# Optimization experiments

Hardware: AMD Instinct MI355X
Metric: run time of the kernel (lower is better)

The kernel has to match this reference:

```python
import jax, jax.numpy as jnp
import numpy as np

BATCH, ENC_IN, D_MODEL, D_STATE = 16, 256, 256, 16


def _mamba_params(key, d, d_conv, prefix):
    di = 2 * d  # expand = 2
    dtr = max(d // 16, 1)  # dt_rank = ceil(d_model/16)
    ks = jax.random.split(key, 6)
    return {
        prefix + '_in_w': jax.random.normal(ks[0], (2 * di, d), jnp.float32) * 0.02,
        prefix + '_conv_w': jax.random.normal(ks[1], (di, d_conv), jnp.float32) * 0.1,
        prefix + '_conv_b': jnp.zeros((di,), jnp.float32),
        prefix + '_xproj_w': jax.random.normal(ks[2], (dtr + 2 * D_STATE, di), jnp.float32) * 0.02,
        prefix + '_dt_w': jax.random.normal(ks[3], (di, dtr), jnp.float32) * 0.02,
        prefix + '_dt_b': jax.random.normal(ks[4], (di,), jnp.float32) * 0.02,
        prefix + '_Alog': jnp.log(jnp.broadcast_to(jnp.arange(1, D_STATE + 1, dtype=jnp.float32), (di, D_STATE))),
        prefix + '_Dp': jnp.ones((di,), jnp.float32),
        prefix + '_out_w': jax.random.normal(ks[5], (d, di), jnp.float32) * 0.02,
    }


def setup_inputs() -> dict:
    key = jax.random.key(0)
    k0, k1, k2, k3 = jax.random.split(key, 4)
    inp = {
        'x': jax.random.normal(k0, (BATCH, ENC_IN, D_MODEL), jnp.float32),
        'ln_g': jnp.ones((D_MODEL,), jnp.float32),
        'ln_b': jnp.zeros((D_MODEL,), jnp.float32),
    }
    inp.update(_mamba_params(k1, D_MODEL, 1, 'mf'))  # channel mixer fwd, d_conv=1
    inp.update(_mamba_params(k2, D_MODEL, 1, 'mb'))  # channel mixer bwd, d_conv=1
    inp.update(_mamba_params(k3, ENC_IN, 4, 'tm'))   # time mixer, d_conv=4
    return inp


def _mamba(x, in_w, conv_w, conv_b, xproj_w, dt_w, dt_b, Alog, Dp, out_w):
    # x: [B, L, d]  -> standard mamba_ssm Mamba block forward
    B, L, d = x.shape
    di = in_w.shape[0] // 2
    dtr = dt_w.shape[1]
    ds = D_STATE
    xz = x @ in_w.T                      # [B, L, 2*di]
    xs, z = xz[..., :di], xz[..., di:]
    # causal depthwise conv1d (pad left d_conv-1, truncate to L)
    K = conv_w.shape[1]
    xp = jnp.pad(xs, ((0, 0), (K - 1, 0), (0, 0)))
    xs = sum(conv_w[:, k] * xp[:, k:k + L, :] for k in range(K)) + conv_b
    xs = jax.nn.silu(xs)
    x_dbl = xs @ xproj_w.T               # [B, L, dtr + 2*ds]
    dt = x_dbl[..., :dtr]
    Bm = x_dbl[..., dtr:dtr + ds]        # [B, L, ds]
    Cm = x_dbl[..., dtr + ds:]           # [B, L, ds]
    delta = jax.nn.softplus(dt @ dt_w.T + dt_b)          # [B, L, di]
    A = -jnp.exp(Alog)                                   # [di, ds]
    dA = jnp.exp(delta[..., None] * A)                   # [B, L, di, ds]
    dBx = delta[..., None] * Bm[:, :, None, :] * xs[..., None]

    def step(h, inp):
        dAt, dBxt, Ct = inp              # [B,di,ds],[B,di,ds],[B,ds]
        h = dAt * h + dBxt
        return h, jnp.einsum('bds,bs->bd', h, Ct)

    h0 = jnp.zeros((B, di, ds), x.dtype)
    _, ys = jax.lax.scan(step, h0, (dA.transpose(1, 0, 2, 3), dBx.transpose(1, 0, 2, 3), Cm.transpose(1, 0, 2)))
    y = ys.transpose(1, 0, 2) + Dp * xs  # [B, L, di]
    y = y * jax.nn.silu(z)
    return y @ out_w.T                   # [B, L, d]


def _ln(x, g, b, eps=1e-5):
    m = x.mean(-1, keepdims=True)
    v = jnp.mean((x - m) ** 2, axis=-1, keepdims=True)
    return (x - m) / jnp.sqrt(v + eps) * g + b


def reference(x, ln_g, ln_b,
              mf_in_w, mf_conv_w, mf_conv_b, mf_xproj_w, mf_dt_w, mf_dt_b, mf_Alog, mf_Dp, mf_out_w,
              mb_in_w, mb_conv_w, mb_conv_b, mb_xproj_w, mb_dt_w, mb_dt_b, mb_Alog, mb_Dp, mb_out_w,
              tm_in_w, tm_conv_w, tm_conv_b, tm_xproj_w, tm_dt_w, tm_dt_b, tm_Alog, tm_Dp, tm_out_w):
    # BiMamba channel mixer
    y_f = _mamba(x, mf_in_w, mf_conv_w, mf_conv_b, mf_xproj_w, mf_dt_w, mf_dt_b, mf_Alog, mf_Dp, mf_out_w)
    y_b = _mamba(jnp.flip(x, axis=1), mb_in_w, mb_conv_w, mb_conv_b, mb_xproj_w, mb_dt_w, mb_dt_b, mb_Alog, mb_Dp, mb_out_w)
    y0 = y_f + jnp.flip(y_b, axis=1) + x
    y0 = _ln(y0, ln_g, ln_b)             # note: source uses norm1 both times
    # time mixer over the feature dimension
    y1 = y0.transpose(0, 2, 1)           # [B, d_model, enc_in]
    y1 = _mamba(y1, tm_in_w, tm_conv_w, tm_conv_b, tm_xproj_w, tm_dt_w, tm_dt_b, tm_Alog, tm_Dp, tm_out_w)
    y1 = y1.transpose(0, 2, 1)
    y2 = y1 * y0 + x
    return _ln(y2, ln_g, ln_b)
```

## Files before the change

### kernel.cpp

```cpp
#include <hip/hip_runtime.h>
#include <hip/hip_bf16.h>

typedef unsigned short u16;
typedef unsigned int   u32;

typedef short frag8 __attribute__((ext_vector_type(8)));
typedef float f32x4 __attribute__((ext_vector_type(4)));
typedef u16   u16x8 __attribute__((ext_vector_type(8)));
typedef u16   u16x4 __attribute__((ext_vector_type(4)));

__device__ __forceinline__ float bfb2f(u16 u) {
    return __uint_as_float(((u32)u) << 16);
}
__device__ __forceinline__ u16 f2bf(float v) {
    const u32 u = __float_as_uint(v);
    return (u16)((u + 0x7FFFu + ((u >> 16) & 1u)) >> 16);
}
__device__ __forceinline__ float silu_(float x) { return x / (1.f + __expf(-x)); }
__device__ __forceinline__ float softplus_fast(float x) {
    return (x > 20.f) ? x : __logf(1.f + __expf(x));
}
__device__ __forceinline__ void gload_lds16(const void* g, void* l) {
    __builtin_amdgcn_global_load_lds(
        (const __attribute__((address_space(1))) void*)g,
        (__attribute__((address_space(3))) void*)l, 16, 0, 0);
}

struct Cvt {
    const void* src[30];
    int dstoff[30];
    int n[30];
    int bstart[31];
};

__global__ __launch_bounds__(256) void convert_k(Cvt c, const u32* probe,
                                                 float* dst, u16* dstb) {
    const bool isb = (*probe != 0x3F800000u);
    const int bi = blockIdx.x;
    int i = 0;
    while (i < 29 && bi >= c.bstart[i + 1]) ++i;
    const int e = (bi - c.bstart[i]) * 256 + (int)threadIdx.x;
    if (e >= c.n[i]) return;
    const float v = isb ? bfb2f(((const u16*)c.src[i])[e])
                        : ((const float*)c.src[i])[e];
    dst[c.dstoff[i] + e]  = v;
    dstb[c.dstoff[i] + e] = f2bf(v);
}

__global__ __launch_bounds__(256, 4) void gemm1_fb_k(
    const u16* __restrict__ Xbf,
    const u16* __restrict__ Wf, const u16* __restrict__ Wb,
    const float* __restrict__ cwf, const float* __restrict__ cbf,
    const float* __restrict__ cwb, const float* __restrict__ cbb,
    u16* __restrict__ XSb_f, u16* __restrict__ XST_f, u16* __restrict__ ZST_f,
    u16* __restrict__ XSb_b, u16* __restrict__ XST_b, u16* __restrict__ ZST_b)
{
    __shared__ u16 Bs[16384];
    u16 (*tile)[136] = (u16(*)[136])Bs;

    const int br = blockIdx.x >> 4;
    const int n0 = (blockIdx.x & 15) * 64;
    const u16* W = br ? Wb : Wf;
    const float* cw = br ? cwb : cwf;
    const float* cb = br ? cbb : cbf;
    u16* XSb = br ? XSb_b : XSb_f;
    u16* XST = br ? XST_b : XST_f;
    u16* ZST = br ? ZST_b : ZST_f;

    const int t = threadIdx.x;
    const int wave = t >> 6, lane = t & 63;
    const int l15 = lane & 15, quad = lane >> 4;
    const int mblk = blockIdx.y * 128;

    {
        const char* Wp = (const char*)(W + (size_t)n0 * 256);
        const int lane16 = lane * 16;
        #pragma unroll
        for (int j = 0; j < 8; ++j) {
            const int s  = wave * 8 + j;
            const int Lb = s * 1024 + lane16;
            const int Ob = Lb ^ (((Lb >> 9) & 7) << 4);
            gload_lds16(Wp + Ob, (char*)Bs + Lb);
        }
    }
    asm volatile("s_waitcnt vmcnt(0)" ::: "memory");
    __syncthreads();

    const int m0w = mblk + wave * 32;
    const u16* arow0 = Xbf + (size_t)(m0w + l15) * 256 + quad * 8;
    const u16* arow1 = arow0 + 16 * 256;
    f32x4 acc[2][4] = {};
    #pragma unroll
    for (int kk = 0; kk < 8; ++kk) {
        const frag8 a0 = *(const frag8*)(arow0 + kk * 32);
        const frag8 a1 = *(const frag8*)(arow1 + kk * 32);
        #pragma unroll
        for (int ni = 0; ni < 4; ++ni) {
            const int bb = ((ni * 16 + l15) * 512 + kk * 64 + quad * 16)
                         ^ ((l15 & 7) << 4);
            const frag8 b = *(const frag8*)((const char*)Bs + bb);
            acc[0][ni] = __builtin_amdgcn_mfma_f32_16x16x32_bf16(a0, b, acc[0][ni], 0, 0, 0);
            acc[1][ni] = __builtin_amdgcn_mfma_f32_16x16x32_bf16(a1, b, acc[1][ni], 0, 0, 0);
        }
    }
    __syncthreads();

    const bool isx = (n0 < 512);
    #pragma unroll
    for (int mi = 0; mi < 2; ++mi) {
        #pragma unroll
        for (int ni = 0; ni < 4; ++ni) {
            const int n = n0 + ni * 16 + l15;
            #pragma unroll
            for (int r = 0; r < 4; ++r) {
                const int ml = wave * 32 + mi * 16 + quad * 4 + r;
                const int m  = mblk + ml;
                const float v = acc[mi][ni][r];
                const float s = isx ? silu_(fmaf(cw[n], v, cb[n])) : silu_(v);
                const u16 sb = f2bf(s);
                if (isx) XSb[(size_t)m * 512 + n] = sb;
                tile[ni * 16 + l15][ml] = sb;
            }
        }
    }
    __syncthreads();

    const int b2 = mblk >> 8;
    const int l0 = mblk & 255;
    const int rown = t >> 2;
    const int cc  = (t & 3) * 32;
    const int dg = isx ? (n0 + rown) : (n0 - 512 + rown);
    u16* dst = (isx ? XST : ZST) + ((size_t)(b2 * 512 + dg)) * 256 + l0 + cc;
    #pragma unroll
    for (int p = 0; p < 4; ++p)
        *(u16x8*)(dst + p * 8) = *(const u16x8*)&tile[rown][cc + p * 8];
}

__global__ __launch_bounds__(256, 4) void gemm1_tm_k(
    const u16* __restrict__ Ab, const u16* __restrict__ Bbg,
    float* __restrict__ TMRAW, u16* __restrict__ ZST)
{
    __shared__ u16 Bs[16384];
    u16 (*tile)[136] = (u16(*)[136])Bs;

    const int t = threadIdx.x;
    const int wave = t >> 6, lane = t & 63;
    const int l15 = lane & 15, quad = lane >> 4;
    const int mblk = blockIdx.y * 128;
    const int n0 = blockIdx.x * 64;

    {
        const char* Wp = (const char*)(Bbg + (size_t)n0 * 256);
        const int lane16 = lane * 16;
        #pragma unroll
        for (int j = 0; j < 8; ++j) {
            const int s  = wave * 8 + j;
            const int Lb = s * 1024 + lane16;
            const int Ob = Lb ^ (((Lb >> 9) & 7) << 4);
            gload_lds16(Wp + Ob, (char*)Bs + Lb);
        }
    }
    asm volatile("s_waitcnt vmcnt(0)" ::: "memory");
    __syncthreads();

    const int m0w = mblk + wave * 32;
    const u16* arow0 = Ab + (size_t)(m0w + l15) * 256 + quad * 8;
    const u16* arow1 = arow0 + 16 * 256;
    f32x4 acc[2][4] = {};
    #pragma unroll
    for (int kk = 0; kk < 8; ++kk) {
        const frag8 a0 = *(const frag8*)(arow0 + kk * 32);
        const frag8 a1 = *(const frag8*)(arow1 + kk * 32);
        #pragma unroll
        for (int ni = 0; ni < 4; ++ni) {
            const int bb = ((ni * 16 + l15) * 512 + kk * 64 + quad * 16)
                         ^ ((l15 & 7) << 4);
            const frag8 b = *(const frag8*)((const char*)Bs + bb);
            acc[0][ni] = __builtin_amdgcn_mfma_f32_16x16x32_bf16(a0, b, acc[0][ni], 0, 0, 0);
            acc[1][ni] = __builtin_amdgcn_mfma_f32_16x16x32_bf16(a1, b, acc[1][ni], 0, 0, 0);
        }
    }

    const bool isx = (n0 < 512);
    if (isx) {
        #pragma unroll
        for (int mi = 0; mi < 2; ++mi) {
            #pragma unroll
            for (int ni = 0; ni < 4; ++ni) {
                const int n = n0 + ni * 16 + l15;
                #pragma unroll
                for (int r = 0; r < 4; ++r) {
                    const int m = mblk + wave * 32 + mi * 16 + quad * 4 + r;
                    TMRAW[(size_t)m * 512 + n] = acc[mi][ni][r];
                }
            }
        }
    } else {
        __syncthreads();
        #pragma unroll
        for (int mi = 0; mi < 2; ++mi) {
            #pragma unroll
            for (int ni = 0; ni < 4; ++ni) {
                #pragma unroll
                for (int r = 0; r < 4; ++r) {
                    const int ml = wave * 32 + mi * 16 + quad * 4 + r;
                    tile[ni * 16 + l15][ml] = f2bf(silu_(acc[mi][ni][r]));
                }
            }
        }
        __syncthreads();
        const int b2 = mblk >> 8;
        const int l0 = mblk & 255;
        const int rown = t >> 2;
        const int cc  = (t & 3) * 32;
        u16* dst = ZST + ((size_t)(b2 * 512 + (n0 - 512) + rown)) * 256 + l0 + cc;
        #pragma unroll
        for (int p = 0; p < 4; ++p)
            *(u16x8*)(dst + p * 8) = *(const u16x8*)&tile[rown][cc + p * 8];
    }
}

__global__ __launch_bounds__(256, 2) void gemm_x_k(
    const u16* __restrict__ A0, const u16* __restrict__ B0, u16* __restrict__ O0,
    const u16* __restrict__ A1, const u16* __restrict__ B1, u16* __restrict__ O1)
{
    const int br = blockIdx.z;
    const u16* Ab = br ? A1 : A0;
    const u16* Bb = br ? B1 : B0;
    u16* out = br ? O1 : O0;
    const int t = threadIdx.x;
    const int wave = t >> 6, lane = t & 63;
    const int l15 = lane & 15, quad = lane >> 4;
    const int m0 = blockIdx.y * 64 + wave * 16;
    const int n0 = blockIdx.x * 16;
    const u16* arow = Ab + (size_t)(m0 + l15) * 512 + quad * 8;
    const u16* brow = Bb + (size_t)(n0 + l15) * 512 + quad * 8;

    frag8 a[16], b[16];
    #pragma unroll
    for (int kk = 0; kk < 16; ++kk) {
        a[kk] = *(const frag8*)(arow + kk * 32);
        b[kk] = *(const frag8*)(brow + kk * 32);
    }
    f32x4 acc0 = {}, acc1 = {};
    #pragma unroll
    for (int kk = 0; kk < 16; kk += 2) {
        acc0 = __builtin_amdgcn_mfma_f32_16x16x32_bf16(a[kk],     b[kk],     acc0, 0, 0, 0);
        acc1 = __builtin_amdgcn_mfma_f32_16x16x32_bf16(a[kk + 1], b[kk + 1], acc1, 0, 0, 0);
    }
    const f32x4 acc = acc0 + acc1;
    const int n = n0 + l15;
    #pragma unroll
    for (int r = 0; r < 4; ++r) {
        const int m = m0 + quad * 4 + r;
        out[(size_t)m * 48 + n] = f2bf(acc[r]);
    }
}

__global__ __launch_bounds__(256) void gemm_dt_k(
    const u16* __restrict__ A0, const u16* __restrict__ W0,
    const float* __restrict__ bias0, u16* __restrict__ O0,
    const u16* __restrict__ A1, const u16* __restrict__ W1,
    const float* __restrict__ bias1, u16* __restrict__ O1)
{
    __shared__ u16 tile[64][72];
    const int br = blockIdx.z;
    const u16* Ab = br ? A1 : A0;
    const u16* Wt = br ? W1 : W0;
    const float* bias = br ? bias1 : bias0;
    u16* out = br ? O1 : O0;

    const int t = threadIdx.x;
    const int wave = t >> 6, lane = t & 63;
    const int l15 = lane & 15, quad = lane >> 4;
    const int mblk = blockIdx.y * 64;
    const int m0 = mblk + wave * 16;
    const int n0 = blockIdx.x * 64;
    f32x4 acc[4] = {};
    frag8 a;
    #pragma unroll
    for (int j = 0; j < 8; ++j) a[j] = 0;
    if (quad < 2) a = *(const frag8*)(Ab + (size_t)(m0 + l15) * 48 + quad * 8);
    #pragma unroll
    for (int ni = 0; ni < 4; ++ni) {
        frag8 b;
        #pragma unroll
        for (int j = 0; j < 8; ++j) b[j] = 0;
        if (quad < 2) b = *(const frag8*)(Wt + (size_t)(n0 + ni * 16 + l15) * 16 + quad * 8);
        acc[ni] = __builtin_amdgcn_mfma_f32_16x16x32_bf16(a, b, acc[ni], 0, 0, 0);
    }
    #pragma unroll
    for (int ni = 0; ni < 4; ++ni) {
        const int n = n0 + ni * 16 + l15;
        #pragma unroll
        for (int r = 0; r < 4; ++r) {
            const int m = m0 + quad * 4 + r;
            tile[n - n0][m - mblk] = f2bf(softplus_fast(acc[ni][r] + bias[n]));
        }
    }
    __syncthreads();
    const int b  = mblk >> 8;
    const int l0 = mblk & 255;
    const int rown = t >> 2;
    const int chk  = (t & 3) * 16;
    u16* dst = out + ((size_t)(b * 512 + n0 + rown)) * 256 + l0 + chk;
    *(u16x8*)dst       = *(const u16x8*)&tile[rown][chk];
    *(u16x8*)(dst + 8) = *(const u16x8*)&tile[rown][chk + 8];
}

__global__ __launch_bounds__(256, 2) void gemm_o_k(
    const u16* __restrict__ A0, const u16* __restrict__ B0, float* __restrict__ O0,
    const u16* __restrict__ A1, const u16* __restrict__ B1, float* __restrict__ O1)
{
    const int br = blockIdx.z;
    const u16* Ab = br ? A1 : A0;
    const u16* Bb = br ? B1 : B0;
    float* out = br ? O1 : O0;
    const int t = threadIdx.x;
    const int wave = t >> 6, lane = t & 63;
    const int l15 = lane & 15, quad = lane >> 4;
    const int m0 = blockIdx.y * 64 + wave * 16;
    const int n0 = blockIdx.x * 32;
    const u16* arow = Ab + (size_t)(m0 + l15) * 512 + quad * 8;
    const u16* brow = Bb + (size_t)(n0 + l15) * 512 + quad * 8;

    frag8 a[16];
    #pragma unroll
    for (int kk = 0; kk < 16; ++kk)
        a[kk] = *(const frag8*)(arow + kk * 32);
    frag8 b[16][2];
    #pragma unroll
    for (int kk = 0; kk < 16; ++kk)
        #pragma unroll
        for (int ni = 0; ni < 2; ++ni)
            b[kk][ni] = *(const frag8*)(brow + (size_t)ni * 16 * 512 + kk * 32);

    f32x4 acc0[2] = {}, acc1[2] = {};
    #pragma unroll
    for (int kk = 0; kk < 16; kk += 2) {
        #pragma unroll
        for (int ni = 0; ni < 2; ++ni) {
            acc0[ni] = __builtin_amdgcn_mfma_f32_16x16x32_bf16(a[kk],     b[kk][ni],     acc0[ni], 0, 0, 0);
            acc1[ni] = __builtin_amdgcn_mfma_f32_16x16x32_bf16(a[kk + 1], b[kk + 1][ni], acc1[ni], 0, 0, 0);
        }
    }
    #pragma unroll
    for (int ni = 0; ni < 2; ++ni) {
        const f32x4 acc = acc0[ni] + acc1[ni];
        const int n = n0 + ni * 16 + l15;
        #pragma unroll
        for (int r = 0; r < 4; ++r) {
            const int m = m0 + quad * 4 + r;
            out[(size_t)m * 256 + n] = acc[r];
        }
    }
}

__global__ __launch_bounds__(256) void conv4t_k(
    const float* __restrict__ raw, const float* __restrict__ cw, const float* __restrict__ cb,
    u16* __restrict__ XSb, u16* __restrict__ XST)
{
    __shared__ u16 tile[64][72];
    const int b  = blockIdx.y;
    const int c0 = blockIdx.x * 64;
    const int cl = threadIdx.x & 63;
    const int seg = threadIdx.x >> 6;
    const int c = c0 + cl;
    const int tq = blockIdx.z * 64;
    const int tp0 = tq + seg * 16;
    const float w0 = cw[c * 4 + 0], w1 = cw[c * 4 + 1];
    const float w2 = cw[c * 4 + 2], w3 = cw[c * 4 + 3];
    const float bias = cb[c];
    float r3 = 0.f, r2 = 0.f, r1 = 0.f;
    if (tp0 > 0) {
        r3 = raw[((size_t)(b * 256 + tp0 - 3)) * 512 + c];
        r2 = raw[((size_t)(b * 256 + tp0 - 2)) * 512 + c];
        r1 = raw[((size_t)(b * 256 + tp0 - 1)) * 512 + c];
    }
    #pragma unroll
    for (int i = 0; i < 16; ++i) {
        const int tp = tp0 + i;
        const float cur = raw[((size_t)(b * 256 + tp)) * 512 + c];
        float acc = fmaf(w0, r3, bias);
        acc = fmaf(w1, r2, acc);
        acc = fmaf(w2, r1, acc);
        acc = fmaf(w3, cur, acc);
        const u16 sb = f2bf(silu_(acc));
        XSb[((size_t)(b * 256 + tp)) * 512 + c] = sb;
        tile[cl][tp - tq] = sb;
        r3 = r2; r2 = r1; r1 = cur;
    }
    __syncthreads();
    const int row = threadIdx.x >> 2;
    const int ch  = (threadIdx.x & 3) * 16;
    u16* dst = XST + ((size_t)(b * 512 + c0 + row)) * 256 + tq + ch;
    #pragma unroll
    for (int j = 0; j < 4; ++j)
        *(u16x4*)(dst + j * 4) = *(const u16x4*)&tile[row][ch + j * 4];
}

struct ScanSet {
    const u16 *xst, *zst, *dlt, *xdblb;
    const float *Alog, *Dp;
    u16* Y;
};

__global__ __launch_bounds__(256) void scan_fused_k(ScanSet s0, ScanSet s1, int branchStart)
{
    __shared__ float Ps[4354];
    __shared__ float Es[4354];
    const int br  = (blockIdx.x >= (u32)branchStart) ? 1 : 0;
    const ScanSet S = br ? s1 : s0;
    const int rev = br;
    const int bi2 = blockIdx.x - br * branchStart;
    const int b  = bi2 >> 6;
    const int d0 = (bi2 & 63) << 3;
    const int g  = threadIdx.x >> 3;
    const int cl = threadIdx.x & 7;
    const int d  = d0 + cl;

    bool fast = true;
    #pragma unroll
    for (int s = 0; s < 16; ++s) {
        const float a = -__expf(S.Alog[d * 16 + s]);
        fast &= (fabsf(a + (float)(s + 1)) < 1e-3f);
    }

    const size_t crow = ((size_t)(b * 512 + d)) * 256;
    const int lbase = rev ? (248 - g * 8) : (g * 8);
    const u16x8 xs8 = *(const u16x8*)(S.xst + crow + lbase);
    const u16x8 dl8 = *(const u16x8*)(S.dlt + crow + lbase);

    float h[16], P[16];
    #pragma unroll
    for (int s = 0; s < 16; ++s) { h[s] = 0.f; P[s] = 1.f; }
    float e1prod = 1.f;

    #pragma unroll
    for (int i = 0; i < 8; ++i) {
        const int j = rev ? (7 - i) : i;
        const int l = lbase + j;
        const size_t row = (size_t)(b * 256 + l);
        const float dl = bfb2f(dl8[j]);
        const float xv = bfb2f(xs8[j]);
        const u16x8 bv0 = *(const u16x8*)(S.xdblb + row * 48 + 16);
        const u16x8 bv1 = *(const u16x8*)(S.xdblb + row * 48 + 24);
        const float dlx = dl * xv;
        if (fast) {
            const float e1 = __expf(-dl);
            e1prod *= e1;
            const float e2 = e1 * e1, e4 = e2 * e2, e8 = e4 * e4;
            float pw[16];
            pw[0] = e1;        pw[1] = e2;        pw[2] = e2 * e1;   pw[3] = e4;
            pw[4] = e4 * e1;   pw[5] = e4 * e2;   pw[6] = e4 * pw[2]; pw[7] = e8;
            pw[8] = e8 * e1;   pw[9] = e8 * e2;   pw[10] = e8 * pw[2]; pw[11] = e8 * e4;
            pw[12] = e8 * pw[4]; pw[13] = e8 * pw[5]; pw[14] = e8 * pw[6]; pw[15] = e8 * e8;
            #pragma unroll
            for (int s = 0; s < 8; ++s)
                h[s] = fmaf(pw[s], h[s], dlx * bfb2f(bv0[s]));
            #pragma unroll
            for (int s = 8; s < 16; ++s)
                h[s] = fmaf(pw[s], h[s], dlx * bfb2f(bv1[s - 8]));
        } else {
            #pragma unroll
            for (int s = 0; s < 16; ++s) {
                const float As = -__expf(S.Alog[d * 16 + s]);
                const float dA = __expf(dl * As);
                P[s] *= dA;
                const float Bv = bfb2f((s < 8) ? bv0[s] : bv1[s - 8]);
                h[s] = fmaf(dA, h[s], dlx * Bv);
            }
        }
    }
    if (fast) {
        const float e1 = e1prod;
        const float e2 = e1 * e1, e4 = e2 * e2, e8 = e4 * e4;
        P[0] = e1;        P[1] = e2;        P[2] = e2 * e1;   P[3] = e4;
        P[4] = e4 * e1;   P[5] = e4 * e2;   P[6] = e4 * P[2]; P[7] = e8;
        P[8] = e8 * e1;   P[9] = e8 * e2;   P[10] = e8 * P[2]; P[11] = e8 * e4;
        P[12] = e8 * P[4]; P[13] = e8 * P[5]; P[14] = e8 * P[6]; P[15] = e8 * e8;
    }
    const int pbx = (g * 8 + cl) * 17;
    #pragma unroll
    for (int s = 0; s < 16; ++s) { Ps[pbx + s] = P[s]; Es[pbx + s] = h[s]; }
    __syncthreads();

    if (threadIdx.x < 128) {
        const int cl2 = threadIdx.x >> 4, s2 = threadIdx.x & 15;
        float hh = 0.f;
        #pragma unroll
        for (int gg = 0; gg < 32; ++gg) {
            const int o = (gg * 8 + cl2) * 17 + s2;
            const float tmp = Es[o];
            Es[o] = hh;
            hh = fmaf(Ps[o], hh, tmp);
        }
    }
    __syncthreads();

    #pragma unroll
    for (int s = 0; s < 16; ++s) h[s] = Es[pbx + s];
    const float Dpd = S.Dp[d];
    const u16x8 zs8 = *(const u16x8*)(S.zst + crow + lbase);
    #pragma unroll
    for (int i = 0; i < 8; ++i) {
        const int j = rev ? (7 - i) : i;
        const int l = lbase + j;
        const size_t row = (size_t)(b * 256 + l);
        const float dl = bfb2f(dl8[j]);
        const float xv = bfb2f(xs8[j]);
        const float zv = bfb2f(zs8[j]);
        const u16x8 bv0 = *(const u16x8*)(S.xdblb + row * 48 + 16);
        const u16x8 bv1 = *(const u16x8*)(S.xdblb + row * 48 + 24);
        const u16x8 cv0 = *(const u16x8*)(S.xdblb + row * 48 + 32);
        const u16x8 cv1 = *(const u16x8*)(S.xdblb + row * 48 + 40);
        const float dlx = dl * xv;
        float a0 = 0.f, a1 = 0.f, a2 = 0.f, a3 = 0.f;
        if (fast) {
            const float e1 = __expf(-dl);
            const float e2 = e1 * e1, e4 = e2 * e2, e8 = e4 * e4;
            float pw[16];
            pw[0] = e1;        pw[1] = e2;        pw[2] = e2 * e1;   pw[3] = e4;
            pw[4] = e4 * e1;   pw[5] = e4 * e2;   pw[6] = e4 * pw[2]; pw[7] = e8;
            pw[8] = e8 * e1;   pw[9] = e8 * e2;   pw[10] = e8 * pw[2]; pw[11] = e8 * e4;
            pw[12] = e8 * pw[4]; pw[13] = e8 * pw[5]; pw[14] = e8 * pw[6]; pw[15] = e8 * e8;
            #pragma unroll
            for (int s = 0; s < 16; ++s) {
                const float Bv = bfb2f((s < 8) ? bv0[s] : bv1[s - 8]);
                const float Cv = bfb2f((s < 8) ? cv0[s] : cv1[s - 8]);
                h[s] = fmaf(pw[s], h[s], dlx * Bv);
                const float hv = h[s] * Cv;
                if ((s & 3) == 0) a0 += hv;
                else if ((s & 3) == 1) a1 += hv;
                else if ((s & 3) == 2) a2 += hv;
                else a3 += hv;
            }
        } else {
            #pragma unroll
            for (int s = 0; s < 16; ++s) {
                const float As = -__expf(S.Alog[d * 16 + s]);
                const float dA = __expf(dl * As);
                const float Bv = bfb2f((s < 8) ? bv0[s] : bv1[s - 8]);
                const float Cv = bfb2f((s < 8) ? cv0[s] : cv1[s - 8]);
                h[s] = fmaf(dA, h[s], dlx * Bv);
                const float hv = h[s] * Cv;
                if ((s & 3) == 0) a0 += hv;
                else if ((s & 3) == 1) a1 += hv;
                else if ((s & 3) == 2) a2 += hv;
                else a3 += hv;
            }
        }
        const float acc = (a0 + a1) + (a2 + a3);
        S.Y[row * 512 + d] = f2bf((acc + Dpd * xv) * zv);
    }
}

__global__ __launch_bounds__(256) void combine_ln_k(
    const float* __restrict__ YF, const float* __restrict__ YB,
    const float* __restrict__ X, const float* __restrict__ g, const float* __restrict__ bb,
    float* __restrict__ Y0)
{
    const int m = blockIdx.x;
    const int c = threadIdx.x;
    const float v = YF[(size_t)m * 256 + c]
                  + YB[(size_t)m * 256 + c]
                  + X[(size_t)m * 256 + c];
    float s1 = v, s2 = v * v;
    #pragma unroll
    for (int off = 32; off > 0; off >>= 1) {
        s1 += __shfl_down(s1, off);
        s2 += __shfl_down(s2, off);
    }
    __shared__ float p1[4], p2[4];
    const int wave = c >> 6;
    if ((c & 63) == 0) { p1[wave] = s1; p2[wave] = s2; }
    __syncthreads();
    const float t1 = (p1[0] + p1[1]) + (p1[2] + p1[3]);
    const float t2 = (p2[0] + p2[1]) + (p2[2] + p2[3]);
    const float mean = t1 * (1.f / 256.f);
    const float var  = t2 * (1.f / 256.f) - mean * mean;
    const float inv  = rsqrtf(var + 1e-5f);
    Y0[(size_t)m * 256 + c] = (v - mean) * inv * g[c] + bb[c];
}

__global__ __launch_bounds__(256) void transpose_cast_k(
    const float* __restrict__ Y0, u16* __restrict__ Y0T)
{
    __shared__ float tile[64][65];
    const int b  = blockIdx.z;
    const int l0 = blockIdx.x * 64, c0 = blockIdx.y * 64;
    const int tc = threadIdx.x & 63;
    const int tr = threadIdx.x >> 6;
    #pragma unroll
    for (int j = 0; j < 16; ++j) {
        const int r = tr * 16 + j;
        tile[r][tc] = Y0[((size_t)(b * 256 + l0 + r)) * 256 + c0 + tc];
    }
    __syncthreads();
    #pragma unroll
    for (int j = 0; j < 16; ++j) {
        const int r = tr * 16 + j;
        Y0T[((size_t)(b * 256 + c0 + r)) * 256 + l0 + tc] = f2bf(tile[tc][r]);
    }
}

__global__ __launch_bounds__(256) void final_ln_k(
    const float* __restrict__ TMOUT, const float* __restrict__ Y0,
    const float* __restrict__ X, const float* __restrict__ g, const float* __restrict__ bb,
    float* __restrict__ out)
{
    const int m = blockIdx.x;
    const int c = threadIdx.x;
    const int b = m >> 8, l = m & 255;
    const float y1 = TMOUT[((size_t)(b * 256 + c)) * 256 + l];
    const float v = fmaf(y1, Y0[(size_t)m * 256 + c], X[(size_t)m * 256 + c]);
    float s1 = v, s2 = v * v;
    #pragma unroll
    for (int off = 32; off > 0; off >>= 1) {
        s1 += __shfl_down(s1, off);
        s2 += __shfl_down(s2, off);
    }
    __shared__ float p1[4], p2[4];
    const int wave = c >> 6;
    if ((c & 63) == 0) { p1[wave] = s1; p2[wave] = s2; }
    __syncthreads();
    const float t1 = (p1[0] + p1[1]) + (p1[2] + p1[3]);
    const float t2 = (p2[0] + p2[1]) + (p2[2] + p2[3]);
    const float mean = t1 * (1.f / 256.f);
    const float var  = t2 * (1.f / 256.f) - mean * mean;
    const float inv  = rsqrtf(var + 1e-5f);
    out[(size_t)m * 256 + c] = (v - mean) * inv * g[c] + bb[c];
}

extern "C" void kernel_launch(void* const* d_in, const int* in_sizes, int n_in,
                              void* d_out, int out_size, void* d_ws, size_t ws_size,
                              hipStream_t stream)
{
    float* ws = (float*)d_ws;

    Cvt c;
    int off = 0, blocks = 0;
    int doff[30];
    for (int i = 0; i < 30; ++i) {
        c.src[i]    = d_in[i];
        c.dstoff[i] = off;
        doff[i]     = off;
        c.n[i]      = in_sizes[i];
        c.bstart[i] = blocks;
        off    += in_sizes[i];
        blocks += (in_sizes[i] + 255) / 256;
    }
    c.bstart[30] = blocks;
    const int offa = (off + 7) & ~7;
    float* PARF = ws;
    u16*   PARB = (u16*)(ws + offa);
    float* ACT0 = ws + offa + offa / 2;

    convert_k<<<dim3(blocks), dim3(256), 0, stream>>>(c, (const u32*)d_in[1], PARF, PARB);

    auto P  = [&](int base, int o) -> const float* { return PARF + doff[base + o]; };
    auto Pb = [&](int base, int o) -> const u16*   { return PARB + doff[base + o]; };
    const float* X   = P(0, 0);
    const u16*   Xbf = Pb(0, 0);
    const float* lng = P(1, 0);
    const float* lnb = P(2, 0);

    u16* XSb_f   = (u16*)ACT0;
    u16* XSb_b   = XSb_f + 2097152;
    u16* XST_f   = XSb_b + 2097152;
    u16* XST_b   = XST_f + 2097152;
    u16* ZST_f   = XST_b + 2097152;
    u16* ZST_b   = ZST_f + 2097152;
    u16* DLT_f   = ZST_b + 2097152;
    u16* DLT_b   = DLT_f + 2097152;
    u16* Ybf_f   = DLT_b + 2097152;
    u16* Ybf_b   = Ybf_f + 2097152;
    u16* XDBLb_f = Ybf_b + 2097152;
    u16* XDBLb_b = XDBLb_f + 196608;
    u16* Y0T     = XDBLb_b + 196608;
    float* Y0    = (float*)(Y0T + 1048576);
    float* YF    = Y0 + 1048576;
    float* YB    = YF + 1048576;
    float* TMRAW = YB + 1048576;
    float* TMOUT = TMRAW + 2097152;

    const dim3 blk(256);
    const int mf = 3, mb = 12, tm = 21;

    gemm1_fb_k<<<dim3(32, 32), blk, 0, stream>>>(
        Xbf, Pb(mf, 0), Pb(mb, 0),
        P(mf, 1), P(mf, 2), P(mb, 1), P(mb, 2),
        XSb_f, XST_f, ZST_f, XSb_b, XST_b, ZST_b);
    gemm_x_k<<<dim3(3, 64, 2), blk, 0, stream>>>(
        XSb_f, Pb(mf, 3), XDBLb_f, XSb_b, Pb(mb, 3), XDBLb_b);
    gemm_dt_k<<<dim3(8, 64, 2), blk, 0, stream>>>(
        XDBLb_f, Pb(mf, 4), P(mf, 5), DLT_f,
        XDBLb_b, Pb(mb, 4), P(mb, 5), DLT_b);
    {
        ScanSet s0 { XST_f, ZST_f, DLT_f, XDBLb_f, P(mf, 6), P(mf, 7), Ybf_f };
        ScanSet s1 { XST_b, ZST_b, DLT_b, XDBLb_b, P(mb, 6), P(mb, 7), Ybf_b };
        scan_fused_k<<<dim3(2048), blk, 0, stream>>>(s0, s1, 1024);
    }
    gemm_o_k<<<dim3(8, 64, 2), blk, 0, stream>>>(
        Ybf_f, Pb(mf, 8), YF, Ybf_b, Pb(mb, 8), YB);

    combine_ln_k<<<dim3(4096), blk, 0, stream>>>(YF, YB, X, lng, lnb, Y0);
    transpose_cast_k<<<dim3(4, 4, 16), blk, 0, stream>>>(Y0, Y0T);

    gemm1_tm_k<<<dim3(16, 32), blk, 0, stream>>>(Y0T, Pb(tm, 0), TMRAW, ZST_f);
    conv4t_k<<<dim3(8, 16, 4), blk, 0, stream>>>(TMRAW, P(tm, 1), P(tm, 2), XSb_f, XST_f);
    gemm_x_k<<<dim3(3, 64, 1), blk, 0, stream>>>(
        XSb_f, Pb(tm, 3), XDBLb_f, XSb_f, Pb(tm, 3), XDBLb_f);
    gemm_dt_k<<<dim3(8, 64, 1), blk, 0, stream>>>(
        XDBLb_f, Pb(tm, 4), P(tm, 5), DLT_f,
        XDBLb_f, Pb(tm, 4), P(tm, 5), DLT_f);
    {
        ScanSet t0 { XST_f, ZST_f, DLT_f, XDBLb_f, P(tm, 6), P(tm, 7), Ybf_f };
        scan_fused_k<<<dim3(1024), blk, 0, stream>>>(t0, t0, 2048);
    }
    gemm_o_k<<<dim3(8, 64, 1), blk, 0, stream>>>(
        Ybf_f, Pb(tm, 8), TMOUT, Ybf_f, Pb(tm, 8), TMOUT);

    final_ln_k<<<dim3(4096), blk, 0, stream>>>(TMOUT, Y0, X, lng, lnb, (float*)d_out);
}
```

Before: 283.2 us.

## Stage GEMM operands in swizzled LDS and fold transpose into combine LN

gemm_x_k now loads its whole A and B tiles into XOR-swizzled LDS with direct global-to-LDS loads, instead of holding per-lane register fragments. gemm_o_k stages B in LDS and doubles the M tile per block so each B fragment is reused across two A rows, with the launch grid halved to match. The separate transpose_cast kernel is removed; combine_ln_k writes the transposed bf16 copy directly, saving a launch and a re-read of Y0. In exchange, the transposed store in combine_ln_k is strided and uncoalesced, and gemm_x_k's 80KB LDS footprint limits occupancy.

```diff
diff --git a/kernel.cpp b/kernel.cpp
--- a/kernel.cpp
+++ b/kernel.cpp
@@ -224,6 +224,7 @@
     const u16* __restrict__ A0, const u16* __restrict__ B0, u16* __restrict__ O0,
     const u16* __restrict__ A1, const u16* __restrict__ B1, u16* __restrict__ O1)
 {
+    __shared__ char AB[81920];
     const int br = blockIdx.z;
     const u16* Ab = br ? A1 : A0;
     const u16* Bb = br ? B1 : B0;
@@ -231,30 +232,43 @@
     const int t = threadIdx.x;
     const int wave = t >> 6, lane = t & 63;
     const int l15 = lane & 15, quad = lane >> 4;
-    const int m0 = blockIdx.y * 64 + wave * 16;
+    const int mblk = blockIdx.y * 64;
     const int n0 = blockIdx.x * 16;
-    const u16* arow = Ab + (size_t)(m0 + l15) * 512 + quad * 8;
-    const u16* brow = Bb + (size_t)(n0 + l15) * 512 + quad * 8;
-
-    frag8 a[16], b[16];
+
+    {
+        const char* Ap = (const char*)(Ab + (size_t)mblk * 512);
+        const char* Bp = (const char*)(Bb + (size_t)n0 * 512);
+        const int lane16 = lane * 16;
+        #pragma unroll
+        for (int j = 0; j < 16; ++j) {
+            const int Lb = (wave * 16 + j) * 1024 + lane16;
+            const int Ob = Lb ^ (((Lb >> 10) & 7) << 4);
+            gload_lds16(Ap + Ob, AB + Lb);
+        }
+        #pragma unroll
+        for (int j = 0; j < 4; ++j) {
+            const int Lb = (wave * 4 + j) * 1024 + lane16;
+            const int Ob = Lb ^ (((Lb >> 10) & 7) << 4);
+            gload_lds16(Bp + Ob, AB + 65536 + Lb);
+        }
+    }
+    asm volatile("s_waitcnt vmcnt(0)" ::: "memory");
+    __syncthreads();
+
+    f32x4 acc = {};
     #pragma unroll
     for (int kk = 0; kk < 16; ++kk) {
-        a[kk] = *(const frag8*)(arow + kk * 32);
-        b[kk] = *(const frag8*)(brow + kk * 32);
-    }
-    f32x4 acc0 = {}, acc1 = {};
-    #pragma unroll
-    for (int kk = 0; kk < 16; kk += 2) {
-        acc0 = __builtin_amdgcn_mfma_f32_16x16x32_bf16(a[kk],     b[kk],     acc0, 0, 0, 0);
-        acc1 = __builtin_amdgcn_mfma_f32_16x16x32_bf16(a[kk + 1], b[kk + 1], acc1, 0, 0, 0);
-    }
-    const f32x4 acc = acc0 + acc1;
+        const int aoff = ((wave * 16 + l15) * 1024 + kk * 64 + quad * 16) ^ ((l15 & 7) << 4);
+        const int boff = 65536 + ((l15 * 1024 + kk * 64 + quad * 16) ^ ((l15 & 7) << 4));
+        const frag8 a = *(const frag8*)(AB + aoff);
+        const frag8 b = *(const frag8*)(AB + boff);
+        acc = __builtin_amdgcn_mfma_f32_16x16x32_bf16(a, b, acc, 0, 0, 0);
+    }
     const int n = n0 + l15;
-    #pragma unroll
-    for (int r = 0; r < 4; ++r) {
-        const int m = m0 + quad * 4 + r;
-        out[(size_t)m * 48 + n] = f2bf(acc[r]);
-    }
+    const int m0 = mblk + wave * 16;
+    #pragma unroll
+    for (int r = 0; r < 4; ++r)
+        out[(size_t)(m0 + quad * 4 + r) * 48 + n] = f2bf(acc[r]);
 }
 
 __global__ __launch_bounds__(256) void gemm_dt_k(
@@ -308,10 +322,11 @@
     *(u16x8*)(dst + 8) = *(const u16x8*)&tile[rown][chk + 8];
 }
 
-__global__ __launch_bounds__(256, 2) void gemm_o_k(
+__global__ __launch_bounds__(256, 4) void gemm_o_k(
     const u16* __restrict__ A0, const u16* __restrict__ B0, float* __restrict__ O0,
     const u16* __restrict__ A1, const u16* __restrict__ B1, float* __restrict__ O1)
 {
+    __shared__ char Bs[32768];
     const int br = blockIdx.z;
     const u16* Ab = br ? A1 : A0;
     const u16* Bb = br ? B1 : B0;
@@ -319,39 +334,48 @@
     const int t = threadIdx.x;
     const int wave = t >> 6, lane = t & 63;
     const int l15 = lane & 15, quad = lane >> 4;
-    const int m0 = blockIdx.y * 64 + wave * 16;
+    const int mblk = blockIdx.y * 128;
     const int n0 = blockIdx.x * 32;
-    const u16* arow = Ab + (size_t)(m0 + l15) * 512 + quad * 8;
-    const u16* brow = Bb + (size_t)(n0 + l15) * 512 + quad * 8;
-
-    frag8 a[16];
-    #pragma unroll
-    for (int kk = 0; kk < 16; ++kk)
-        a[kk] = *(const frag8*)(arow + kk * 32);
-    frag8 b[16][2];
-    #pragma unroll
-    for (int kk = 0; kk < 16; ++kk)
-        #pragma unroll
-        for (int ni = 0; ni < 2; ++ni)
-            b[kk][ni] = *(const frag8*)(brow + (size_t)ni * 16 * 512 + kk * 32);
-
-    f32x4 acc0[2] = {}, acc1[2] = {};
-    #pragma unroll
-    for (int kk = 0; kk < 16; kk += 2) {
+
+    {
+        const char* Bp = (const char*)(Bb + (size_t)n0 * 512);
+        const int lane16 = lane * 16;
+        #pragma unroll
+        for (int j = 0; j < 8; ++j) {
+            const int Lb = (wave * 8 + j) * 1024 + lane16;
+            const int Ob = Lb ^ (((Lb >> 10) & 7) << 4);
+            gload_lds16(Bp + Ob, Bs + Lb);
+        }
+    }
+    asm volatile("s_waitcnt vmcnt(0)" ::: "memory");
+    __syncthreads();
+
+    const int m0w = mblk + wave * 32;
+    const u16* arow0 = Ab + (size_t)(m0w + l15) * 512 + quad * 8;
+    const u16* arow1 = arow0 + 16 * 512;
+    f32x4 acc[2][2] = {};
+    #pragma unroll
+    for (int kk = 0; kk < 16; ++kk) {
+        const frag8 a0 = *(const frag8*)(arow0 + kk * 32);
+        const frag8 a1 = *(const frag8*)(arow1 + kk * 32);
         #pragma unroll
         for (int ni = 0; ni < 2; ++ni) {
-            acc0[ni] = __builtin_amdgcn_mfma_f32_16x16x32_bf16(a[kk],     b[kk][ni],     acc0[ni], 0, 0, 0);
-            acc1[ni] = __builtin_amdgcn_mfma_f32_16x16x32_bf16(a[kk + 1], b[kk + 1][ni], acc1[ni], 0, 0, 0);
-        }
-    }
-    #pragma unroll
-    for (int ni = 0; ni < 2; ++ni) {
-        const f32x4 acc = acc0[ni] + acc1[ni];
-        const int n = n0 + ni * 16 + l15;
-        #pragma unroll
-        for (int r = 0; r < 4; ++r) {
-            const int m = m0 + quad * 4 + r;
-            out[(size_t)m * 256 + n] = acc[r];
+            const int boff = ((ni * 16 + l15) * 1024 + kk * 64 + quad * 16) ^ ((l15 & 7) << 4);
+            const frag8 b = *(const frag8*)(Bs + boff);
+            acc[0][ni] = __builtin_amdgcn_mfma_f32_16x16x32_bf16(a0, b, acc[0][ni], 0, 0, 0);
+            acc[1][ni] = __builtin_amdgcn_mfma_f32_16x16x32_bf16(a1, b, acc[1][ni], 0, 0, 0);
+        }
+    }
+    #pragma unroll
+    for (int mi = 0; mi < 2; ++mi) {
+        #pragma unroll
+        for (int ni = 0; ni < 2; ++ni) {
+            const int n = n0 + ni * 16 + l15;
+            #pragma unroll
+            for (int r = 0; r < 4; ++r) {
+                const int m = mblk + wave * 32 + mi * 16 + quad * 4 + r;
+                out[(size_t)m * 256 + n] = acc[mi][ni][r];
+            }
         }
     }
 }
@@ -558,7 +582,7 @@
 __global__ __launch_bounds__(256) void combine_ln_k(
     const float* __restrict__ YF, const float* __restrict__ YB,
     const float* __restrict__ X, const float* __restrict__ g, const float* __restrict__ bb,
-    float* __restrict__ Y0)
+    float* __restrict__ Y0, u16* __restrict__ Y0T)
 {
     const int m = blockIdx.x;
     const int c = threadIdx.x;
@@ -580,28 +604,10 @@
     const float mean = t1 * (1.f / 256.f);
     const float var  = t2 * (1.f / 256.f) - mean * mean;
     const float inv  = rsqrtf(var + 1e-5f);
-    Y0[(size_t)m * 256 + c] = (v - mean) * inv * g[c] + bb[c];
-}
-
-__global__ __launch_bounds__(256) void transpose_cast_k(
-    const float* __restrict__ Y0, u16* __restrict__ Y0T)
-{
-    __shared__ float tile[64][65];
-    const int b  = blockIdx.z;
-    const int l0 = blockIdx.x * 64, c0 = blockIdx.y * 64;
-    const int tc = threadIdx.x & 63;
-    const int tr = threadIdx.x >> 6;
-    #pragma unroll
-    for (int j = 0; j < 16; ++j) {
-        const int r = tr * 16 + j;
-        tile[r][tc] = Y0[((size_t)(b * 256 + l0 + r)) * 256 + c0 + tc];
-    }
-    __syncthreads();
-    #pragma unroll
-    for (int j = 0; j < 16; ++j) {
-        const int r = tr * 16 + j;
-        Y0T[((size_t)(b * 256 + c0 + r)) * 256 + l0 + tc] = f2bf(tile[tc][r]);
-    }
+    const float o = (v - mean) * inv * g[c] + bb[c];
+    Y0[(size_t)m * 256 + c] = o;
+    const int b2 = m >> 8, l = m & 255;
+    Y0T[((size_t)(b2 * 256 + c)) * 256 + l] = f2bf(o);
 }
 
 __global__ __launch_bounds__(256) void final_ln_k(
@@ -701,11 +707,10 @@
         ScanSet s1 { XST_b, ZST_b, DLT_b, XDBLb_b, P(mb, 6), P(mb, 7), Ybf_b };
         scan_fused_k<<<dim3(2048), blk, 0, stream>>>(s0, s1, 1024);
     }
-    gemm_o_k<<<dim3(8, 64, 2), blk, 0, stream>>>(
+    gemm_o_k<<<dim3(8, 32, 2), blk, 0, stream>>>(
         Ybf_f, Pb(mf, 8), YF, Ybf_b, Pb(mb, 8), YB);
 
-    combine_ln_k<<<dim3(4096), blk, 0, stream>>>(YF, YB, X, lng, lnb, Y0);
-    transpose_cast_k<<<dim3(4, 4, 16), blk, 0, stream>>>(Y0, Y0T);
+    combine_ln_k<<<dim3(4096), blk, 0, stream>>>(YF, YB, X, lng, lnb, Y0, Y0T);
 
     gemm1_tm_k<<<dim3(16, 32), blk, 0, stream>>>(Y0T, Pb(tm, 0), TMRAW, ZST_f);
     conv4t_k<<<dim3(8, 16, 4), blk, 0, stream>>>(TMRAW, P(tm, 1), P(tm, 2), XSb_f, XST_f);
@@ -718,7 +723,7 @@
         ScanSet t0 { XST_f, ZST_f, DLT_f, XDBLb_f, P(tm, 6), P(tm, 7), Ybf_f };
         scan_fused_k<<<dim3(1024), blk, 0, stream>>>(t0, t0, 2048);
     }
-    gemm_o_k<<<dim3(8, 64, 1), blk, 0, stream>>>(
+    gemm_o_k<<<dim3(8, 32, 1), blk, 0, stream>>>(
         Ybf_f, Pb(tm, 8), TMOUT, Ybf_f, Pb(tm, 8), TMOUT);
 
     final_ln_k<<<dim3(4096), blk, 0, stream>>>(TMOUT, Y0, X, lng, lnb, (float*)d_out);
```

After: 265.4 us, median of 2. 1.07x faster.
